# Kernel tuning notes

Hardware: AMD Instinct MI355X
Metric: run time of the kernel (lower is better)

The kernel has to match this reference:

```python
import jax, jax.numpy as jnp
import numpy as np

EPS = 1.1920929e-07  # torch F.rms_norm default eps for fp32
HEADS = 16
KV_HEADS = 4
HEAD_DIM = 64
WINDOW = 1024
NEG = -1e30

def rms_norm(x):
    return x * jax.lax.rsqrt(jnp.mean(x * x, axis=-1, keepdims=True) + EPS)

def rope_freqs(L, head_dim):
    half = head_dim // 2
    inv_freq = 1.0 / (10000.0 ** (jnp.arange(half, dtype=jnp.float32) / half))
    f = jnp.outer(jnp.arange(L, dtype=jnp.float32), inv_freq)  # (L, half)
    return jnp.concatenate([f, f], axis=-1)  # (L, head_dim)

def apply_rope(x, freqs):
    # x: (B, L, H, D), freqs: (L, D)
    cos = jnp.cos(freqs)[None, :, None, :]
    sin = jnp.sin(freqs)[None, :, None, :]
    half = x.shape[-1] // 2
    x1, x2 = x[..., :half], x[..., half:]
    return jnp.concatenate([
        x1 * cos[..., :half] - x2 * sin[..., half:],
        x1 * sin[..., :half] + x2 * cos[..., half:],
    ], axis=-1)

def setup_inputs() -> dict:
    key = jax.random.key(0)
    k1, k2, k3, k4 = jax.random.split(key, 4)
    B, L, D = 2, 2048, 1024
    x = jax.random.normal(k1, (B, L, D), dtype=jnp.float32)
    w_qkv = jax.random.normal(k2, (1536, D), dtype=jnp.float32) * 0.02
    w_out = jax.random.normal(k3, (D, D), dtype=jnp.float32) * 0.02
    reset_mask = jax.random.randint(k4, (B, L), 0, 2) == 1
    return {"x": x, "w_qkv": w_qkv, "w_out": w_out, "reset_mask": reset_mask}

def reference(x, w_qkv, w_out, reset_mask):
    B, L, D = x.shape
    residual = x
    h = rms_norm(x)
    qkv = h @ w_qkv.T  # (B, L, 1536)
    q_dim = HEADS * HEAD_DIM
    kv_dim = KV_HEADS * HEAD_DIM
    q = qkv[..., :q_dim].reshape(B, L, HEADS, HEAD_DIM)
    k = qkv[..., q_dim:q_dim + kv_dim].reshape(B, L, KV_HEADS, HEAD_DIM)
    v = qkv[..., q_dim + kv_dim:].reshape(B, L, KV_HEADS, HEAD_DIM)
    q = rms_norm(q)
    k = rms_norm(k)
    freqs = rope_freqs(L, HEAD_DIM)
    q = apply_rope(q, freqs)
    k = apply_rope(k, freqs)
    groups = HEADS // KV_HEADS
    k = jnp.repeat(k, groups, axis=2)  # (B, L, H, D)
    v = jnp.repeat(v, groups, axis=2)
    q = q.transpose(0, 2, 1, 3)  # (B, H, L, D)
    k = k.transpose(0, 2, 1, 3)
    v = v.transpose(0, 2, 1, 3)
    # mask: same document & causal & sliding window
    seg = jnp.cumsum(reset_mask.astype(jnp.int32), axis=1)  # (B, L)
    same_doc = seg[:, :, None] == seg[:, None, :]  # (B, L, L)
    idx = jnp.arange(L)
    dist = idx[:, None] - idx[None, :]
    cw = (dist >= 0) & (dist < WINDOW)  # (L, L)
    mask = same_doc & cw[None]  # (B, L, L)
    scale = 1.0 / np.sqrt(HEAD_DIM)
    scores = jnp.einsum('bhqd,bhkd->bhqk', q, k) * scale
    scores = jnp.where(mask[:, None, :, :], scores, NEG)
    probs = jax.nn.softmax(scores, axis=-1)
    y = jnp.einsum('bhqk,bhkd->bhqd', probs, v)
    y = y.transpose(0, 2, 1, 3).reshape(B, L, D)
    return residual + y @ w_out.T
```

## Files before the change

kernel.cpp:

```cpp
#include <hip/hip_runtime.h>

typedef __attribute__((ext_vector_type(8))) short short8;
typedef __attribute__((ext_vector_type(4))) float f32x4;
typedef __attribute__((ext_vector_type(4))) unsigned short us4;

__device__ __forceinline__ unsigned short f2bf(float f){
  unsigned int u = __float_as_uint(f);
  u = (u + 0x7FFFu + ((u >> 16) & 1u)) >> 16;
  return (unsigned short)u;
}
__device__ __forceinline__ float bf2f(unsigned short h){
  return __uint_as_float(((unsigned int)h) << 16);
}

__global__ __launch_bounds__(256)
void cvt_w(const float* __restrict__ wq, const float* __restrict__ wo,
           unsigned short* __restrict__ wqb, unsigned short* __restrict__ wob){
  int i = blockIdx.x * 256 + threadIdx.x;
  const int n1 = 1536 * 1024 / 4;
  float4 v = (i < n1) ? ((const float4*)wq)[i] : ((const float4*)wo)[i - n1];
  us4 o = { f2bf(v.x), f2bf(v.y), f2bf(v.z), f2bf(v.w) };
  if (i < n1) ((us4*)wqb)[i] = o;
  else        ((us4*)wob)[i - n1] = o;
}

__global__ __launch_bounds__(256)
void rmsnorm_x(const float* __restrict__ x, unsigned short* __restrict__ h){
  int row = blockIdx.x, t = threadIdx.x;
  float4 v = ((const float4*)(x + (size_t)row * 1024))[t];
  float ss = v.x*v.x + v.y*v.y + v.z*v.z + v.w*v.w;
  #pragma unroll
  for (int m = 1; m < 64; m <<= 1) ss += __shfl_xor(ss, m);
  __shared__ float wsum[4];
  if ((t & 63) == 0) wsum[t >> 6] = ss;
  __syncthreads();
  float tot = wsum[0] + wsum[1] + wsum[2] + wsum[3];
  float sc = rsqrtf(tot * (1.f/1024.f) + 1.1920929e-07f);
  us4 o = { f2bf(v.x*sc), f2bf(v.y*sc), f2bf(v.z*sc), f2bf(v.w*sc) };
  *(us4*)(h + (size_t)row * 1024 + t * 4) = o;
}

template<bool BF_OUT, bool RES>
__global__ __launch_bounds__(256)
void gemm_nt(const unsigned short* __restrict__ A, const unsigned short* __restrict__ B,
             int M, int N, int K, float* __restrict__ Cf, unsigned short* __restrict__ Cb,
             const float* __restrict__ resid){
  constexpr int RS = 72;
  __shared__ short As[128 * RS];
  __shared__ short Bs[128 * RS];
  const int nbn = N >> 7;
  const int bm = blockIdx.x / nbn;
  const int bn = blockIdx.x % nbn;
  const int t = threadIdx.x;
  const int lane = t & 63;
  const int wv = t >> 6;
  const int wm = (wv >> 1) * 64, wn = (wv & 1) * 64;
  const int lr = lane & 15, lg = lane >> 4;

  f32x4 acc[4][4];
  #pragma unroll
  for (int m = 0; m < 4; m++)
    #pragma unroll
    for (int n = 0; n < 4; n++) acc[m][n] = (f32x4){0.f,0.f,0.f,0.f};

  const unsigned short* Ab = A + (size_t)(bm * 128) * K;
  const unsigned short* Bb = B + (size_t)(bn * 128) * K;

  for (int kt = 0; kt < K; kt += 64) {
    #pragma unroll
    for (int i = 0; i < 4; i++) {
      int slot = t + i * 256;
      int row = slot >> 3, cg = slot & 7;
      short8 va = *(const short8*)(Ab + (size_t)row * K + kt + cg * 8);
      short8 vb = *(const short8*)(Bb + (size_t)row * K + kt + cg * 8);
      *(short8*)&As[row * RS + cg * 8] = va;
      *(short8*)&Bs[row * RS + cg * 8] = vb;
    }
    __syncthreads();
    #pragma unroll
    for (int kk = 0; kk < 2; kk++) {
      short8 af[4], bfr[4];
      #pragma unroll
      for (int m = 0; m < 4; m++) af[m] = *(const short8*)&As[(wm + m*16 + lr)*RS + kk*32 + lg*8];
      #pragma unroll
      for (int n = 0; n < 4; n++) bfr[n] = *(const short8*)&Bs[(wn + n*16 + lr)*RS + kk*32 + lg*8];
      #pragma unroll
      for (int m = 0; m < 4; m++)
        #pragma unroll
        for (int n = 0; n < 4; n++)
          acc[m][n] = __builtin_amdgcn_mfma_f32_16x16x32_bf16(af[m], bfr[n], acc[m][n], 0, 0, 0);
    }
    __syncthreads();
  }
  #pragma unroll
  for (int m = 0; m < 4; m++)
    #pragma unroll
    for (int n = 0; n < 4; n++)
      #pragma unroll
      for (int r = 0; r < 4; r++) {
        int grow = bm*128 + wm + m*16 + lg*4 + r;
        int gcol = bn*128 + wn + n*16 + lr;
        size_t idx = (size_t)grow * N + gcol;
        if (BF_OUT) { Cb[idx] = f2bf(acc[m][n][r]); }
        else {
          float v = acc[m][n][r];
          if (RES) v += resid[idx];
          Cf[idx] = v;
        }
      }
}

__global__ __launch_bounds__(256)
void post_qkv(const unsigned short* __restrict__ qkv,
              unsigned short* __restrict__ Qb, unsigned short* __restrict__ Kb,
              unsigned short* __restrict__ Vt){
  int w = blockIdx.x * 4 + (threadIdx.x >> 6);
  int lane = threadIdx.x & 63;
  int head = w % 24;
  int row  = w / 24;
  int b = row >> 11, pos = row & 2047;
  int off = head < 16 ? head * 64 : (head < 20 ? 1024 + (head-16)*64 : 1280 + (head-20)*64);
  float val = bf2f(qkv[(size_t)row * 1536 + off + lane]);
  if (head < 20) {
    float ss = val * val;
    #pragma unroll
    for (int m = 1; m < 64; m <<= 1) ss += __shfl_xor(ss, m);
    val *= rsqrtf(ss * (1.f/64.f) + 1.1920929e-07f);
    float part = __shfl_xor(val, 32);
    int i = lane & 31;
    float f = (float)pos * exp2f((float)i * (-13.287712379549449f / 32.f));
    float s, c; sincosf(f, &s, &c);
    val = (lane < 32) ? (val * c - part * s) : (part * s + val * c);
  }
  unsigned short o = f2bf(val);
  if (head < 16)      Qb[((size_t)((b*16 + head     )*2048 + pos))*64 + lane] = o;
  else if (head < 20) Kb[((size_t)((b*4  + head - 16)*2048 + pos))*64 + lane] = o;
  else                Vt[((size_t)((b*4  + head - 20)*64 + lane))*2048 + pos] = o;
}

__global__ __launch_bounds__(256)
void compute_lo(const unsigned char* __restrict__ mb, int* __restrict__ lo){
  int b = blockIdx.x, t = threadIdx.x;
  __shared__ int flag_s;
  if (t == 0) flag_s = 0;
  __syncthreads();
  if (t < 64 && (t & 3) != 0 && mb[t] != 0) atomicOr(&flag_s, 1);
  __syncthreads();
  const bool isb = (flag_s != 0);
  const int* mi = (const int*)mb;
  int tmax = 0;
  int mvals[8];
  #pragma unroll
  for (int j = 0; j < 8; j++) {
    int p = t * 8 + j;
    int mv = isb ? (int)mb[b*2048 + p] : mi[b*2048 + p];
    mvals[j] = mv;
    if (mv) tmax = p;
  }
  __shared__ int sm[256];
  sm[t] = tmax;
  __syncthreads();
  for (int offd = 1; offd < 256; offd <<= 1) {
    int v = (t >= offd) ? sm[t - offd] : 0;
    __syncthreads();
    if (t >= offd) sm[t] = max(sm[t], v);
    __syncthreads();
  }
  int run = (t > 0) ? sm[t - 1] : 0;
  #pragma unroll
  for (int j = 0; j < 8; j++) {
    int p = t * 8 + j;
    if (mvals[j]) run = p;
    int l = run, wlo = p - 1023;
    if (wlo > l) l = wlo;
    if (l < 0) l = 0;
    lo[b*2048 + p] = l;
  }
}

__global__ __launch_bounds__(256)
void attn(const unsigned short* __restrict__ Qb, const unsigned short* __restrict__ Kb,
          const unsigned short* __restrict__ Vt, const int* __restrict__ lo,
          unsigned short* __restrict__ Y){
  int blk = blockIdx.x;
  int qt = blk & 31, h = (blk >> 5) & 15, b = blk >> 9;
  int wv = threadIdx.x >> 6, lane = threadIdx.x & 63;
  int lr = lane & 15, lg = lane >> 4;
  int q0 = qt * 64 + wv * 16;
  const unsigned short* Qh = Qb + ((size_t)(b*16 + h)) * 2048 * 64;
  int kvh = h >> 2;
  const unsigned short* Kh = Kb + ((size_t)(b*4 + kvh)) * 2048 * 64;
  const unsigned short* Vh = Vt + ((size_t)(b*4 + kvh)) * 64 * 2048;
  short8 qa0 = *(const short8*)(Qh + (size_t)(q0 + lr) * 64 + lg * 8);
  short8 qa1 = *(const short8*)(Qh + (size_t)(q0 + lr) * 64 + 32 + lg * 8);
  const int* lop = lo + b * 2048 + q0;
  int4 mlv = *(const int4*)(lop + lg * 4);
  int mylo[4] = {mlv.x, mlv.y, mlv.z, mlv.w};
  int kc0 = lop[0] & ~31;
  int kend = q0 + 15;
  f32x4 oacc[4];
  #pragma unroll
  for (int n = 0; n < 4; n++) oacc[n] = (f32x4){0.f,0.f,0.f,0.f};
  float den[4] = {0.f,0.f,0.f,0.f};
  __shared__ __align__(16) short Pl[4][16 * 40];
  short* Pw = Pl[wv];
  for (int kc = kc0; kc <= kend; kc += 32) {
    f32x4 s[2];
    #pragma unroll
    for (int n = 0; n < 2; n++) {
      int kr = kc + n*16 + lr;
      int krl = min(kr, 2047);
      short8 k0 = *(const short8*)(Kh + (size_t)krl * 64 + lg * 8);
      short8 k1 = *(const short8*)(Kh + (size_t)krl * 64 + 32 + lg * 8);
      f32x4 z = (f32x4){0.f,0.f,0.f,0.f};
      z = __builtin_amdgcn_mfma_f32_16x16x32_bf16(qa0, k0, z, 0, 0, 0);
      z = __builtin_amdgcn_mfma_f32_16x16x32_bf16(qa1, k1, z, 0, 0, 0);
      s[n] = z;
    }
    #pragma unroll
    for (int n = 0; n < 2; n++)
      #pragma unroll
      for (int r = 0; r < 4; r++) {
        int krow = kc + n*16 + lr;
        int qrow = q0 + lg*4 + r;
        bool valid = (krow >= mylo[r]) && (krow <= qrow);
        float p = valid ? __expf(s[n][r] * 0.125f) : 0.f;
        den[r] += p;
        Pw[(lg*4 + r) * 40 + n*16 + lr] = (short)f2bf(p);
      }
    short8 pa = *(const short8*)&Pw[lr * 40 + lg * 8];
    int vc = min(kc + lg * 8, 2040);
    #pragma unroll
    for (int n = 0; n < 4; n++) {
      short8 vb = *(const short8*)(Vh + (size_t)(n*16 + lr) * 2048 + vc);
      oacc[n] = __builtin_amdgcn_mfma_f32_16x16x32_bf16(pa, vb, oacc[n], 0, 0, 0);
    }
  }
  #pragma unroll
  for (int r = 0; r < 4; r++)
    #pragma unroll
    for (int m = 1; m < 16; m <<= 1) den[r] += __shfl_xor(den[r], m);
  #pragma unroll
  for (int n = 0; n < 4; n++)
    #pragma unroll
    for (int r = 0; r < 4; r++) {
      int qrow = q0 + lg*4 + r;
      Y[((size_t)(b*2048 + qrow)) * 1024 + h*64 + n*16 + lr] = f2bf(oacc[n][r] / den[r]);
    }
}

extern "C" void kernel_launch(void* const* d_in, const int* in_sizes, int n_in,
                              void* d_out, int out_size, void* d_ws, size_t ws_size,
                              hipStream_t stream){
  const float* x    = (const float*)d_in[0];
  const float* wqkv = (const float*)d_in[1];
  const float* wout = (const float*)d_in[2];
  const unsigned char* mask = (const unsigned char*)d_in[3];
  float* out = (float*)d_out;
  char* ws = (char*)d_ws;
  size_t off = 0;
  auto alloc = [&](size_t bytes) -> void* {
    void* p = ws + off;
    off += (bytes + 255) & ~(size_t)255;
    return p;
  };
  unsigned short* wq_b  = (unsigned short*)alloc((size_t)1536*1024*2);
  unsigned short* wo_b  = (unsigned short*)alloc((size_t)1024*1024*2);
  unsigned short* h_b   = (unsigned short*)alloc((size_t)4096*1024*2);
  unsigned short* qkv_b = (unsigned short*)alloc((size_t)4096*1536*2);
  unsigned short* q_b   = (unsigned short*)alloc((size_t)4096*1024*2);
  unsigned short* k_b   = (unsigned short*)alloc((size_t)4096*256*2);
  unsigned short* vt_b  = (unsigned short*)alloc((size_t)4096*256*2);
  unsigned short* y_b   = (unsigned short*)alloc((size_t)4096*1024*2);
  int* lo               = (int*)alloc((size_t)4096*4);

  cvt_w<<<2560, 256, 0, stream>>>(wqkv, wout, wq_b, wo_b);
  rmsnorm_x<<<4096, 256, 0, stream>>>(x, h_b);
  gemm_nt<true,  false><<<32*12, 256, 0, stream>>>(h_b, wq_b, 4096, 1536, 1024, nullptr, qkv_b, nullptr);
  post_qkv<<<24576, 256, 0, stream>>>(qkv_b, q_b, k_b, vt_b);
  compute_lo<<<2, 256, 0, stream>>>(mask, lo);
  attn<<<1024, 256, 0, stream>>>(q_b, k_b, vt_b, lo, y_b);
  gemm_nt<false, true><<<32*8, 256, 0, stream>>>(y_b, wo_b, 4096, 1024, 1024, out, nullptr, x);
}
```

Baseline: 161.6 us.

## Fuse prep kernels and load GEMM tiles directly into LDS via global_load_lds

Merges weight conversion, input RMSNorm and segment-bound computation into a single launch to cut launch overhead. In the GEMM, tiles are copied from global memory straight into LDS with global_load_lds instead of passing through registers, and the padded LDS row stride is removed. Dropping the padding can cause bank conflicts on fragment reads, which may offset the savings.

```diff
diff --git a/kernel.cpp b/kernel.cpp
--- a/kernel.cpp
+++ b/kernel.cpp
@@ -3,6 +3,9 @@
 typedef __attribute__((ext_vector_type(8))) short short8;
 typedef __attribute__((ext_vector_type(4))) float f32x4;
 typedef __attribute__((ext_vector_type(4))) unsigned short us4;
+
+typedef unsigned int __attribute__((address_space(3))) lds_u32;
+typedef const unsigned int __attribute__((address_space(1))) glb_u32;
 
 __device__ __forceinline__ unsigned short f2bf(float f){
   unsigned int u = __float_as_uint(f);
@@ -14,30 +17,72 @@
 }
 
 __global__ __launch_bounds__(256)
-void cvt_w(const float* __restrict__ wq, const float* __restrict__ wo,
-           unsigned short* __restrict__ wqb, unsigned short* __restrict__ wob){
-  int i = blockIdx.x * 256 + threadIdx.x;
-  const int n1 = 1536 * 1024 / 4;
-  float4 v = (i < n1) ? ((const float4*)wq)[i] : ((const float4*)wo)[i - n1];
-  us4 o = { f2bf(v.x), f2bf(v.y), f2bf(v.z), f2bf(v.w) };
-  if (i < n1) ((us4*)wqb)[i] = o;
-  else        ((us4*)wob)[i - n1] = o;
-}
-
-__global__ __launch_bounds__(256)
-void rmsnorm_x(const float* __restrict__ x, unsigned short* __restrict__ h){
-  int row = blockIdx.x, t = threadIdx.x;
-  float4 v = ((const float4*)(x + (size_t)row * 1024))[t];
-  float ss = v.x*v.x + v.y*v.y + v.z*v.z + v.w*v.w;
-  #pragma unroll
-  for (int m = 1; m < 64; m <<= 1) ss += __shfl_xor(ss, m);
-  __shared__ float wsum[4];
-  if ((t & 63) == 0) wsum[t >> 6] = ss;
+void prep(const float* __restrict__ wq, const float* __restrict__ wo,
+          unsigned short* __restrict__ wqb, unsigned short* __restrict__ wob,
+          const float* __restrict__ x, unsigned short* __restrict__ h,
+          const unsigned char* __restrict__ mb, int* __restrict__ lo){
+  int blk = blockIdx.x;
+  int t = threadIdx.x;
+  if (blk < 2560) {
+    int i = blk * 256 + t;
+    const int n1 = 1536 * 1024 / 4;
+    float4 v = (i < n1) ? ((const float4*)wq)[i] : ((const float4*)wo)[i - n1];
+    us4 o = { f2bf(v.x), f2bf(v.y), f2bf(v.z), f2bf(v.w) };
+    if (i < n1) ((us4*)wqb)[i] = o;
+    else        ((us4*)wob)[i - n1] = o;
+    return;
+  }
+  if (blk < 2560 + 4096) {
+    int row = blk - 2560;
+    float4 v = ((const float4*)(x + (size_t)row * 1024))[t];
+    float ss = v.x*v.x + v.y*v.y + v.z*v.z + v.w*v.w;
+    #pragma unroll
+    for (int m = 1; m < 64; m <<= 1) ss += __shfl_xor(ss, m);
+    __shared__ float wsum[4];
+    if ((t & 63) == 0) wsum[t >> 6] = ss;
+    __syncthreads();
+    float tot = wsum[0] + wsum[1] + wsum[2] + wsum[3];
+    float sc = rsqrtf(tot * (1.f/1024.f) + 1.1920929e-07f);
+    us4 o = { f2bf(v.x*sc), f2bf(v.y*sc), f2bf(v.z*sc), f2bf(v.w*sc) };
+    *(us4*)(h + (size_t)row * 1024 + t * 4) = o;
+    return;
+  }
+  int b = blk - 2560 - 4096;
+  __shared__ int flag_s;
+  if (t == 0) flag_s = 0;
   __syncthreads();
-  float tot = wsum[0] + wsum[1] + wsum[2] + wsum[3];
-  float sc = rsqrtf(tot * (1.f/1024.f) + 1.1920929e-07f);
-  us4 o = { f2bf(v.x*sc), f2bf(v.y*sc), f2bf(v.z*sc), f2bf(v.w*sc) };
-  *(us4*)(h + (size_t)row * 1024 + t * 4) = o;
+  if (t < 64 && (t & 3) != 0 && mb[t] != 0) atomicOr(&flag_s, 1);
+  __syncthreads();
+  const bool isb = (flag_s != 0);
+  const int* mi = (const int*)mb;
+  int tmax = 0;
+  int mvals[8];
+  #pragma unroll
+  for (int j = 0; j < 8; j++) {
+    int p = t * 8 + j;
+    int mv = isb ? (int)mb[b*2048 + p] : mi[b*2048 + p];
+    mvals[j] = mv;
+    if (mv) tmax = p;
+  }
+  __shared__ int sm[256];
+  sm[t] = tmax;
+  __syncthreads();
+  for (int offd = 1; offd < 256; offd <<= 1) {
+    int v = (t >= offd) ? sm[t - offd] : 0;
+    __syncthreads();
+    if (t >= offd) sm[t] = max(sm[t], v);
+    __syncthreads();
+  }
+  int run = (t > 0) ? sm[t - 1] : 0;
+  #pragma unroll
+  for (int j = 0; j < 8; j++) {
+    int p = t * 8 + j;
+    if (mvals[j]) run = p;
+    int l = run, wlo = p - 1023;
+    if (wlo > l) l = wlo;
+    if (l < 0) l = 0;
+    lo[b*2048 + p] = l;
+  }
 }
 
 template<bool BF_OUT, bool RES>
@@ -45,9 +90,8 @@
 void gemm_nt(const unsigned short* __restrict__ A, const unsigned short* __restrict__ B,
              int M, int N, int K, float* __restrict__ Cf, unsigned short* __restrict__ Cb,
              const float* __restrict__ resid){
-  constexpr int RS = 72;
-  __shared__ short As[128 * RS];
-  __shared__ short Bs[128 * RS];
+  __shared__ __align__(16) short As[128 * 64];
+  __shared__ __align__(16) short Bs[128 * 64];
   const int nbn = N >> 7;
   const int bm = blockIdx.x / nbn;
   const int bn = blockIdx.x % nbn;
@@ -56,6 +100,8 @@
   const int wv = t >> 6;
   const int wm = (wv >> 1) * 64, wn = (wv & 1) * 64;
   const int lr = lane & 15, lg = lane >> 4;
+  const int l8 = lane >> 3;
+  const int c8 = (lane & 7) * 8;
 
   f32x4 acc[4][4];
   #pragma unroll
@@ -69,21 +115,21 @@
   for (int kt = 0; kt < K; kt += 64) {
     #pragma unroll
     for (int i = 0; i < 4; i++) {
-      int slot = t + i * 256;
-      int row = slot >> 3, cg = slot & 7;
-      short8 va = *(const short8*)(Ab + (size_t)row * K + kt + cg * 8);
-      short8 vb = *(const short8*)(Bb + (size_t)row * K + kt + cg * 8);
-      *(short8*)&As[row * RS + cg * 8] = va;
-      *(short8*)&Bs[row * RS + cg * 8] = vb;
+      int chunk = wv * 4 + i;
+      int row = chunk * 8 + l8;
+      __builtin_amdgcn_global_load_lds((glb_u32*)(Ab + (size_t)row * K + kt + c8),
+                                       (lds_u32*)&As[chunk * 512], 16, 0, 0);
+      __builtin_amdgcn_global_load_lds((glb_u32*)(Bb + (size_t)row * K + kt + c8),
+                                       (lds_u32*)&Bs[chunk * 512], 16, 0, 0);
     }
     __syncthreads();
     #pragma unroll
     for (int kk = 0; kk < 2; kk++) {
       short8 af[4], bfr[4];
       #pragma unroll
-      for (int m = 0; m < 4; m++) af[m] = *(const short8*)&As[(wm + m*16 + lr)*RS + kk*32 + lg*8];
-      #pragma unroll
-      for (int n = 0; n < 4; n++) bfr[n] = *(const short8*)&Bs[(wn + n*16 + lr)*RS + kk*32 + lg*8];
+      for (int m = 0; m < 4; m++) af[m] = *(const short8*)&As[(wm + m*16 + lr)*64 + kk*32 + lg*8];
+      #pragma unroll
+      for (int n = 0; n < 4; n++) bfr[n] = *(const short8*)&Bs[(wn + n*16 + lr)*64 + kk*32 + lg*8];
       #pragma unroll
       for (int m = 0; m < 4; m++)
         #pragma unroll
@@ -136,46 +182,6 @@
   if (head < 16)      Qb[((size_t)((b*16 + head     )*2048 + pos))*64 + lane] = o;
   else if (head < 20) Kb[((size_t)((b*4  + head - 16)*2048 + pos))*64 + lane] = o;
   else                Vt[((size_t)((b*4  + head - 20)*64 + lane))*2048 + pos] = o;
-}
-
-__global__ __launch_bounds__(256)
-void compute_lo(const unsigned char* __restrict__ mb, int* __restrict__ lo){
-  int b = blockIdx.x, t = threadIdx.x;
-  __shared__ int flag_s;
-  if (t == 0) flag_s = 0;
-  __syncthreads();
-  if (t < 64 && (t & 3) != 0 && mb[t] != 0) atomicOr(&flag_s, 1);
-  __syncthreads();
-  const bool isb = (flag_s != 0);
-  const int* mi = (const int*)mb;
-  int tmax = 0;
-  int mvals[8];
-  #pragma unroll
-  for (int j = 0; j < 8; j++) {
-    int p = t * 8 + j;
-    int mv = isb ? (int)mb[b*2048 + p] : mi[b*2048 + p];
-    mvals[j] = mv;
-    if (mv) tmax = p;
-  }
-  __shared__ int sm[256];
-  sm[t] = tmax;
-  __syncthreads();
-  for (int offd = 1; offd < 256; offd <<= 1) {
-    int v = (t >= offd) ? sm[t - offd] : 0;
-    __syncthreads();
-    if (t >= offd) sm[t] = max(sm[t], v);
-    __syncthreads();
-  }
-  int run = (t > 0) ? sm[t - 1] : 0;
-  #pragma unroll
-  for (int j = 0; j < 8; j++) {
-    int p = t * 8 + j;
-    if (mvals[j]) run = p;
-    int l = run, wlo = p - 1023;
-    if (wlo > l) l = wlo;
-    if (l < 0) l = 0;
-    lo[b*2048 + p] = l;
-  }
 }
 
 __global__ __launch_bounds__(256)
@@ -274,11 +280,9 @@
   unsigned short* y_b   = (unsigned short*)alloc((size_t)4096*1024*2);
   int* lo               = (int*)alloc((size_t)4096*4);
 
-  cvt_w<<<2560, 256, 0, stream>>>(wqkv, wout, wq_b, wo_b);
-  rmsnorm_x<<<4096, 256, 0, stream>>>(x, h_b);
+  prep<<<2560 + 4096 + 2, 256, 0, stream>>>(wqkv, wout, wq_b, wo_b, x, h_b, mask, lo);
   gemm_nt<true,  false><<<32*12, 256, 0, stream>>>(h_b, wq_b, 4096, 1536, 1024, nullptr, qkv_b, nullptr);
   post_qkv<<<24576, 256, 0, stream>>>(qkv_b, q_b, k_b, vt_b);
-  compute_lo<<<2, 256, 0, stream>>>(mask, lo);
   attn<<<1024, 256, 0, stream>>>(q_b, k_b, vt_b, lo, y_b);
   gemm_nt<false, true><<<32*8, 256, 0, stream>>>(y_b, wo_b, 4096, 1024, 1024, out, nullptr, x);
 }
```

New measurement: 164.8 us. Within noise of the previous version (+2.0%).
